# Performance work log

Hardware: AMD Instinct MI355X
Metric: run time of the kernel (lower is better)

## Reference

```python
import jax, jax.numpy as jnp
import numpy as np

B, H, W, C = 16, 32, 32, 512
NUM_HEADS = 8
ATTN_DIM = 512
HEAD_DIM = ATTN_DIM // NUM_HEADS
EPS = 1e-5


def setup_inputs() -> dict:
    key = jax.random.key(0)
    ks = jax.random.split(key, 6)
    s_in = 1.0 / np.sqrt(C)
    s_attn = 1.0 / np.sqrt(ATTN_DIM)
    return {
        "x": jax.random.normal(ks[0], (B, H, W, C), dtype=jnp.float32),
        "gamma": jnp.ones((C,), dtype=jnp.float32),
        "beta": jnp.zeros((C,), dtype=jnp.float32),
        "wq": jax.random.normal(ks[1], (C, ATTN_DIM), dtype=jnp.float32) * s_in,
        "bq": jnp.zeros((ATTN_DIM,), dtype=jnp.float32),
        "wk": jax.random.normal(ks[2], (C, ATTN_DIM), dtype=jnp.float32) * s_in,
        "bk": jnp.zeros((ATTN_DIM,), dtype=jnp.float32),
        "wv": jax.random.normal(ks[3], (C, ATTN_DIM), dtype=jnp.float32) * s_in,
        "bv": jnp.zeros((ATTN_DIM,), dtype=jnp.float32),
        "wo": jax.random.normal(ks[4], (ATTN_DIM, C), dtype=jnp.float32) * s_attn,
        "bo": jnp.zeros((C,), dtype=jnp.float32),
    }


def reference(x, gamma, beta, wq, bq, wk, bk, wv, bv, wo, bo):
    b, h, w, c = x.shape
    t = h * w  # number of spatial tokens
    # GroupNorm with 1 group: normalize over (H, W, C) per sample
    mean = jnp.mean(x, axis=(1, 2, 3), keepdims=True)
    var = jnp.var(x, axis=(1, 2, 3), keepdims=True)
    xn = (x - mean) * jax.lax.rsqrt(var + EPS) * gamma + beta
    xn = xn.reshape(b, t, c)
    # 1x1-conv q/k/v == dense over channel dim; split into heads
    q = (xn @ wq + bq).reshape(b, t, NUM_HEADS, HEAD_DIM)
    k = (xn @ wk + bk).reshape(b, t, NUM_HEADS, HEAD_DIM)
    v = (xn @ wv + bv).reshape(b, t, NUM_HEADS, HEAD_DIM)
    scale = 1.0 / jnp.sqrt(jnp.asarray(HEAD_DIM, dtype=x.dtype))
    scores = jnp.einsum('bqhd,bkhd->bhqk', q, k) * scale
    probs = jax.nn.softmax(scores, axis=-1)
    attn = jnp.einsum('bhqk,bkhd->bqhd', probs, v).reshape(b, t, ATTN_DIM)
    out = attn @ wo + bo
    # Multiplex([None, branch]): residual add, then Reshape([-1, model_dim])
    return x.reshape(b, t, c) + out
```

## Files before the change

### kernel.cpp

```cpp
#include <hip/hip_runtime.h>
#include <hip/hip_bf16.h>

typedef __attribute__((ext_vector_type(8))) short short8;
typedef __attribute__((ext_vector_type(4))) short short4v;
typedef __attribute__((ext_vector_type(4))) float f32x4;

#define B_ 16
#define T_ 1024
#define C_ 512
#define NH 8
#define HD 64

__device__ __forceinline__ short f2bf(float f) {
  union { float f; unsigned u; } v;
  v.f = f;
  unsigned r = v.u + 0x7fffu + ((v.u >> 16) & 1u);
  return (short)(r >> 16);
}

__device__ __forceinline__ short2 pack_bf2(float a, float b) {
  __hip_bfloat162 t = __float22bfloat162_rn(make_float2(a, b));
  short2 r;
  __builtin_memcpy(&r, &t, 4);
  return r;
}

__device__ __forceinline__ float fexp2(float x) {
  float r;
  asm("v_exp_f32 %0, %1" : "=v"(r) : "v"(x));
  return r;
}

__device__ __forceinline__ void gload_lds16(const short* g, short* l) {
  __builtin_amdgcn_global_load_lds(
      (const __attribute__((address_space(1))) void*)g,
      (__attribute__((address_space(3))) void*)l, 16, 0, 0);
}

__global__ __launch_bounds__(256) void stats1_kernel(const float* __restrict__ x,
                                                     float2* __restrict__ partials) {
  int chunk = blockIdx.x;
  int b = blockIdx.y;
  int tid = threadIdx.x;
  const float4* xb = (const float4*)(x + (size_t)b * 524288 + (size_t)chunk * 8192);
  float s = 0.f, s2 = 0.f;
#pragma unroll
  for (int i = 0; i < 8; i++) {
    float4 v = xb[tid + i * 256];
    s  += v.x + v.y + v.z + v.w;
    s2 += v.x * v.x + v.y * v.y + v.z * v.z + v.w * v.w;
  }
  __shared__ float ls[256], ls2[256];
  ls[tid] = s; ls2[tid] = s2;
  __syncthreads();
  for (int o = 128; o > 0; o >>= 1) {
    if (tid < o) { ls[tid] += ls[tid + o]; ls2[tid] += ls2[tid + o]; }
    __syncthreads();
  }
  if (tid == 0) partials[b * 64 + chunk] = make_float2(ls[0], ls2[0]);
}

__global__ __launch_bounds__(64) void stats2_kernel(const float2* __restrict__ partials,
                                                    float* __restrict__ stats) {
  int b = blockIdx.x;
  float2 p = partials[b * 64 + threadIdx.x];
  float s = p.x, s2 = p.y;
#pragma unroll
  for (int off = 1; off < 64; off <<= 1) {
    s  += __shfl_xor(s,  off, 64);
    s2 += __shfl_xor(s2, off, 64);
  }
  if (threadIdx.x == 0) {
    float mean = s * (1.f / 524288.f);
    float var  = s2 * (1.f / 524288.f) - mean * mean;
    stats[b * 2]     = mean;
    stats[b * 2 + 1] = rsqrtf(var + 1e-5f);
  }
}

__global__ __launch_bounds__(256) void norm_kernel(const float* __restrict__ x,
                                                   const float* __restrict__ gamma,
                                                   const float* __restrict__ beta,
                                                   const float* __restrict__ stats,
                                                   short* __restrict__ xn) {
  size_t i4 = (size_t)blockIdx.x * 256 + threadIdx.x;
  float4 v = ((const float4*)x)[i4];
  size_t i = i4 * 4;
  int b = (int)(i >> 19);
  int c = (int)(i & 511);
  float mean = stats[b * 2], rstd = stats[b * 2 + 1];
  short4v o;
  o[0] = f2bf((v.x - mean) * rstd * gamma[c + 0] + beta[c + 0]);
  o[1] = f2bf((v.y - mean) * rstd * gamma[c + 1] + beta[c + 1]);
  o[2] = f2bf((v.z - mean) * rstd * gamma[c + 2] + beta[c + 2]);
  o[3] = f2bf((v.w - mean) * rstd * gamma[c + 3] + beta[c + 3]);
  ((short4v*)xn)[i4] = o;
}

__global__ __launch_bounds__(256) void transpose_w_all(const float* __restrict__ wq,
                                                       const float* __restrict__ wk,
                                                       const float* __restrict__ wv,
                                                       const float* __restrict__ wo,
                                                       short* __restrict__ wqkvT,
                                                       short* __restrict__ woT) {
  int o = blockIdx.x * 256 + threadIdx.x;
  int sel = o >> 18;
  int oo = o & 262143;
  int k = oo >> 9, n = oo & 511;
  const float* w = (sel == 0) ? wq : (sel == 1) ? wk : (sel == 2) ? wv : wo;
  float val = w[oo];
  if (sel < 3) wqkvT[((size_t)(sel * 512 + n)) * 512 + k] = f2bf(val);
  else         woT[(size_t)n * 512 + k] = f2bf(val);
}

__global__ __launch_bounds__(256) void gemm_qkv(const short* __restrict__ A,
                                                const short* __restrict__ Bt,
                                                const float* __restrict__ bq,
                                                const float* __restrict__ bk,
                                                const float* __restrict__ bv,
                                                short* __restrict__ C) {
  __shared__ __align__(16) short As[128 * 32];
  __shared__ __align__(16) short Bs[128 * 32];
  int tid = threadIdx.x;
  int w = tid >> 6, lane = tid & 63;
  int quad = lane >> 4, l16 = lane & 15;
  int mw = (w >> 1) * 64, nw = (w & 1) * 64;
  int seg = (blockIdx.x * 128) >> 9;
  const float* bias = (seg == 0) ? bq : (seg == 1) ? bk : bv;
  float smul = (seg == 0) ? 0.18033688011112042f : 1.0f;
  const short* Atile = A + (size_t)(blockIdx.y * 128) * 512;
  const short* Btile = Bt + (size_t)(blockIdx.x * 128) * 512;
  int srow = (w << 4) + (lane >> 2);
  int scol = (lane & 3) * 8;
  f32x4 acc[4][4] = {};
  for (int k0 = 0; k0 < 512; k0 += 32) {
    __syncthreads();
    gload_lds16(&Atile[(size_t)srow * 512 + k0 + scol],        &As[w * 512]);
    gload_lds16(&Atile[(size_t)(srow + 64) * 512 + k0 + scol], &As[2048 + w * 512]);
    gload_lds16(&Btile[(size_t)srow * 512 + k0 + scol],        &Bs[w * 512]);
    gload_lds16(&Btile[(size_t)(srow + 64) * 512 + k0 + scol], &Bs[2048 + w * 512]);
    __syncthreads();
    short8 af[4], bf[4];
#pragma unroll
    for (int i = 0; i < 4; i++) af[i] = *(const short8*)(&As[(mw + i * 16 + l16) * 32 + quad * 8]);
#pragma unroll
    for (int i = 0; i < 4; i++) bf[i] = *(const short8*)(&Bs[(nw + i * 16 + l16) * 32 + quad * 8]);
#pragma unroll
    for (int mi = 0; mi < 4; mi++)
#pragma unroll
      for (int ni = 0; ni < 4; ni++)
        acc[mi][ni] = __builtin_amdgcn_mfma_f32_16x16x32_bf16(af[mi], bf[ni], acc[mi][ni], 0, 0, 0);
  }
  int m0 = blockIdx.y * 128 + mw;
  int n0 = blockIdx.x * 128 + nw;
#pragma unroll
  for (int mi = 0; mi < 4; mi++)
#pragma unroll
    for (int ni = 0; ni < 4; ni++) {
      int col = n0 + ni * 16 + l16;
      float bval = bias[col & 511];
#pragma unroll
      for (int r = 0; r < 4; r++) {
        int row = m0 + mi * 16 + quad * 4 + r;
        C[(size_t)row * 1536 + col] = f2bf((acc[mi][ni][r] + bval) * smul);
      }
    }
}

__global__ __launch_bounds__(256) void gemm_out(const short* __restrict__ A,
                                                const short* __restrict__ Bt,
                                                const float* __restrict__ bias,
                                                const float* __restrict__ xres,
                                                float* __restrict__ out) {
  __shared__ __align__(16) short As[128 * 32];
  __shared__ __align__(16) short Bs[128 * 32];
  int tid = threadIdx.x;
  int w = tid >> 6, lane = tid & 63;
  int quad = lane >> 4, l16 = lane & 15;
  int mw = (w >> 1) * 64, nw = (w & 1) * 64;
  const short* Atile = A + (size_t)(blockIdx.y * 128) * 512;
  const short* Btile = Bt + (size_t)(blockIdx.x * 128) * 512;
  int srow = (w << 4) + (lane >> 2);
  int scol = (lane & 3) * 8;
  f32x4 acc[4][4] = {};
  for (int k0 = 0; k0 < 512; k0 += 32) {
    __syncthreads();
    gload_lds16(&Atile[(size_t)srow * 512 + k0 + scol],        &As[w * 512]);
    gload_lds16(&Atile[(size_t)(srow + 64) * 512 + k0 + scol], &As[2048 + w * 512]);
    gload_lds16(&Btile[(size_t)srow * 512 + k0 + scol],        &Bs[w * 512]);
    gload_lds16(&Btile[(size_t)(srow + 64) * 512 + k0 + scol], &Bs[2048 + w * 512]);
    __syncthreads();
    short8 af[4], bf[4];
#pragma unroll
    for (int i = 0; i < 4; i++) af[i] = *(const short8*)(&As[(mw + i * 16 + l16) * 32 + quad * 8]);
#pragma unroll
    for (int i = 0; i < 4; i++) bf[i] = *(const short8*)(&Bs[(nw + i * 16 + l16) * 32 + quad * 8]);
#pragma unroll
    for (int mi = 0; mi < 4; mi++)
#pragma unroll
      for (int ni = 0; ni < 4; ni++)
        acc[mi][ni] = __builtin_amdgcn_mfma_f32_16x16x32_bf16(af[mi], bf[ni], acc[mi][ni], 0, 0, 0);
  }
  int m0 = blockIdx.y * 128 + mw;
  int n0 = blockIdx.x * 128 + nw;
#pragma unroll
  for (int mi = 0; mi < 4; mi++)
#pragma unroll
    for (int ni = 0; ni < 4; ni++) {
      int col = n0 + ni * 16 + l16;
      float bval = bias[col];
#pragma unroll
      for (int r = 0; r < 4; r++) {
        int row = m0 + mi * 16 + quad * 4 + r;
        out[(size_t)row * 512 + col] = acc[mi][ni][r] + bval + xres[(size_t)row * 512 + col];
      }
    }
}

__global__ __launch_bounds__(256) void vtrans_kernel(const short* __restrict__ qkv,
                                                     short* __restrict__ vT) {
  int chunk = blockIdx.x;
  int h  = blockIdx.y;
  int b  = blockIdx.z;
  int tid = threadIdx.x;
  __shared__ short TB[128 * 72];
  const short* src = qkv + ((size_t)b * T_ + chunk * 128) * 1536 + 1024 + (size_t)h * 64;
#pragma unroll
  for (int i = 0; i < 4; i++) {
    int idx = tid + i * 256;
    int t = idx >> 3, c = idx & 7;
    *(short8*)(&TB[t * 72 + c * 8]) = *(const short8*)(src + (size_t)t * 1536 + c * 8);
  }
  __syncthreads();
  short* dst = vT + ((size_t)(b * 8 + h) * 64) * 1024 + chunk * 128;
#pragma unroll
  for (int i = 0; i < 4; i++) {
    int idx = tid + i * 256;
    int d = idx >> 4, sc = idx & 15;
    int w2 = sc >> 2, q2 = sc & 3;
    short8 o;
#pragma unroll
    for (int sg = 0; sg < 8; sg++) {
      int half = sg >> 2, r = sg & 3;
      o[sg] = TB[(half * 64 + w2 * 16 + q2 * 4 + r) * 72 + d];
    }
    *(short8*)(dst + (size_t)d * 1024 + sc * 8) = o;
  }
}

__global__ __launch_bounds__(256) void attn_kernel(const short* __restrict__ Q,
                                                   const short* __restrict__ Kmat,
                                                   const short* __restrict__ vTg,
                                                   short* __restrict__ O) {
  int tid = threadIdx.x;
  int w = tid >> 6, lane = tid & 63;
  int quad = lane >> 4, l16 = lane & 15;
  int bh = blockIdx.x;
  int qt = blockIdx.y;
  int b = bh >> 3, h = bh & 7;
  size_t base  = ((size_t)b * T_) * 1536 + (size_t)h * 64;
  size_t vbase = ((size_t)bh * 64) * 1024;
  size_t obase = ((size_t)b * T_) * 512 + (size_t)h * 64;
  int qrow0 = qt * 64;

  __shared__ __align__(16) char smem[32768 + 1024];
  short* KTb[2];
  KTb[0] = (short*)smem;
  KTb[1] = (short*)(smem + 16384);
  float* Lbuf = (float*)smem;
  float* denomL = (float*)(smem + 32768);

  short8 qf0[4], qf1[4];
#pragma unroll
  for (int g = 0; g < 4; g++) {
    const short* qp = Q + base + (size_t)(qrow0 + g * 16 + l16) * 1536 + quad * 8;
    qf0[g] = *(const short8*)qp;
    qf1[g] = *(const short8*)(qp + 32);
  }

  const short* ksrc[4];
#pragma unroll
  for (int n = 0; n < 4; n++) {
    int bk = w * 256 + n * 64 + lane;
    int key = bk >> 3, jc = bk & 7;
    int dcol = jc ^ (key & 7);
    ksrc[n] = Kmat + base + (size_t)key * 1536 + dcol * 8;
  }

  const short* vp0 = vTg + vbase + (size_t)l16 * 1024 + (w * 4 + quad) * 8;

  int l7 = l16 & 7;
  int kA0 = ((w * 16 + l16) * 8 + (quad ^ l7)) * 8;
  int kA1 = ((w * 16 + l16) * 8 + ((quad + 4) ^ l7)) * 8;
  int kB0 = kA0 + 4096;
  int kB1 = kA1 + 4096;

  f32x4 oacc[4][4] = {};
  float lsum[4] = {0.f, 0.f, 0.f, 0.f};

#pragma unroll
  for (int n = 0; n < 4; n++)
    gload_lds16(ksrc[n], KTb[0] + (w * 256 + n * 64) * 8);

#pragma unroll
  for (int t = 0; t < 8; t++) {
    short* KTc = KTb[t & 1];
    short* KTn = KTb[(t + 1) & 1];
    __syncthreads();
    short8 vfr[4];
#pragma unroll
    for (int f = 0; f < 4; f++)
      vfr[f] = *(const short8*)(vp0 + (size_t)f * 16384 + t * 128);
    if (t < 7) {
#pragma unroll
      for (int n = 0; n < 4; n++)
        gload_lds16(ksrc[n] + (size_t)(t + 1) * 196608, KTn + (w * 256 + n * 64) * 8);
    }
    short8 ka0 = *(const short8*)(KTc + kA0);
    short8 ka1 = *(const short8*)(KTc + kA1);
    short8 kb0 = *(const short8*)(KTc + kB0);
    short8 kb1 = *(const short8*)(KTc + kB1);

#pragma unroll
    for (int g = 0; g < 4; g++) {
      f32x4 za = {}, zb = {};
      za = __builtin_amdgcn_mfma_f32_16x16x32_bf16(ka0, qf0[g], za, 0, 0, 0);
      za = __builtin_amdgcn_mfma_f32_16x16x32_bf16(ka1, qf1[g], za, 0, 0, 0);
      zb = __builtin_amdgcn_mfma_f32_16x16x32_bf16(kb0, qf0[g], zb, 0, 0, 0);
      zb = __builtin_amdgcn_mfma_f32_16x16x32_bf16(kb1, qf1[g], zb, 0, 0, 0);
      float pa0 = fexp2(za[0]), pa1 = fexp2(za[1]);
      float pa2 = fexp2(za[2]), pa3 = fexp2(za[3]);
      float pb0 = fexp2(zb[0]), pb1 = fexp2(zb[1]);
      float pb2 = fexp2(zb[2]), pb3 = fexp2(zb[3]);
      lsum[g] += (pa0 + pa1) + (pa2 + pa3) + ((pb0 + pb1) + (pb2 + pb3));
      short2 a01 = pack_bf2(pa0, pa1), a23 = pack_bf2(pa2, pa3);
      short2 b01 = pack_bf2(pb0, pb1), b23 = pack_bf2(pb2, pb3);
      short8 pf;
      pf[0] = a01.x; pf[1] = a01.y; pf[2] = a23.x; pf[3] = a23.y;
      pf[4] = b01.x; pf[5] = b01.y; pf[6] = b23.x; pf[7] = b23.y;
#pragma unroll
      for (int f = 0; f < 4; f++)
        oacc[f][g] = __builtin_amdgcn_mfma_f32_16x16x32_bf16(vfr[f], pf, oacc[f][g], 0, 0, 0);
    }
  }

#pragma unroll
  for (int g = 0; g < 4; g++) {
    lsum[g] += __shfl_xor(lsum[g], 16, 64);
    lsum[g] += __shfl_xor(lsum[g], 32, 64);
  }
  if (quad == 0) {
#pragma unroll
    for (int g = 0; g < 4; g++) denomL[w * 64 + g * 16 + l16] = lsum[g];
  }
  for (int ww = 0; ww < 4; ww++) {
    __syncthreads();
    if (w == ww) {
#pragma unroll
      for (int g = 0; g < 4; g++)
#pragma unroll
        for (int f = 0; f < 4; f++) {
          float* p = &Lbuf[(g * 16 + l16) * 68 + f * 16 + quad * 4];
          if (ww == 0) *(f32x4*)p = oacc[f][g];
          else         *(f32x4*)p = *(f32x4*)p + oacc[f][g];
        }
    }
  }
  __syncthreads();

  int q = tid >> 2, seg = tid & 3;
  float dn = denomL[q] + denomL[64 + q] + denomL[128 + q] + denomL[192 + q];
  float rinv = __frcp_rn(dn);
  const float* row = &Lbuf[q * 68 + seg * 16];
  short8 o0, o1;
#pragma unroll
  for (int i = 0; i < 8; i++) o0[i] = f2bf(row[i] * rinv);
#pragma unroll
  for (int i = 0; i < 8; i++) o1[i] = f2bf(row[8 + i] * rinv);
  short* op = O + obase + (size_t)(qrow0 + q) * 512 + seg * 16;
  *(short8*)op = o0;
  *(short8*)(op + 8) = o1;
}

extern "C" void kernel_launch(void* const* d_in, const int* in_sizes, int n_in,
                              void* d_out, int out_size, void* d_ws, size_t ws_size,
                              hipStream_t stream) {
  const float* x     = (const float*)d_in[0];
  const float* gamma = (const float*)d_in[1];
  const float* beta  = (const float*)d_in[2];
  const float* wq    = (const float*)d_in[3];
  const float* bq    = (const float*)d_in[4];
  const float* wk    = (const float*)d_in[5];
  const float* bk    = (const float*)d_in[6];
  const float* wv    = (const float*)d_in[7];
  const float* bv    = (const float*)d_in[8];
  const float* wo    = (const float*)d_in[9];
  const float* bo    = (const float*)d_in[10];
  float* out = (float*)d_out;

  char* ws = (char*)d_ws;
  const size_t XN_ELEMS = (size_t)B_ * T_ * C_;
  size_t off = 0;
  float* stats = (float*)(ws + off); off += 256;
  float2* partials = (float2*)(ws + off); off += 16 * 64 * sizeof(float2);
  short* xn    = (short*)(ws + off); off += XN_ELEMS * 2;
  short* wqkvT = (short*)(ws + off); off += (size_t)1536 * 512 * 2;
  short* woT   = (short*)(ws + off); off += (size_t)512 * 512 * 2;
  short* qkv   = (short*)(ws + off); off += (size_t)B_ * T_ * 1536 * 2;
  short* vTb   = (short*)(ws + off); off += XN_ELEMS * 2;
  short* ao    = (short*)(ws + off); off += XN_ELEMS * 2;

  stats1_kernel<<<dim3(64, 16), 256, 0, stream>>>(x, partials);
  stats2_kernel<<<16, 64, 0, stream>>>(partials, stats);
  norm_kernel<<<8192, 256, 0, stream>>>(x, gamma, beta, stats, xn);
  transpose_w_all<<<4096, 256, 0, stream>>>(wq, wk, wv, wo, wqkvT, woT);

  gemm_qkv<<<dim3(12, 128), 256, 0, stream>>>(xn, wqkvT, bq, bk, bv, qkv);

  vtrans_kernel<<<dim3(8, 8, 16), 256, 0, stream>>>(qkv, vTb);
  attn_kernel<<<dim3(128, 16), 256, 0, stream>>>(qkv, qkv + 512, vTb, ao);

  gemm_out<<<dim3(4, 128), 256, 0, stream>>>(ao, woT, bo, x, out);
}
```

Baseline: 252.7 us.

## Fuse V transpose into QKV GEMM epilogue and remap attention block order

The QKV GEMM epilogue now writes the V segment straight into the transposed per-head layout the attention kernel reads, so the separate vtrans kernel and its read/write of V go away. The Q/K buffer shrinks to a 1024-wide row stride. The attention kernel also remaps block indices so that consecutive blocks cover different heads and batches, which changes L2 locality. The V stores from the epilogue are scattered 8-byte writes, which may coalesce less well than the old transpose kernel's stores.

```diff
diff --git a/kernel.cpp b/kernel.cpp
--- a/kernel.cpp
+++ b/kernel.cpp
@@ -118,7 +118,8 @@
                                                 const float* __restrict__ bq,
                                                 const float* __restrict__ bk,
                                                 const float* __restrict__ bv,
-                                                short* __restrict__ C) {
+                                                short* __restrict__ C,
+                                                short* __restrict__ vT) {
   __shared__ __align__(16) short As[128 * 32];
   __shared__ __align__(16) short Bs[128 * 32];
   int tid = threadIdx.x;
@@ -153,18 +154,38 @@
   }
   int m0 = blockIdx.y * 128 + mw;
   int n0 = blockIdx.x * 128 + nw;
-#pragma unroll
-  for (int mi = 0; mi < 4; mi++)
-#pragma unroll
-    for (int ni = 0; ni < 4; ni++) {
-      int col = n0 + ni * 16 + l16;
-      float bval = bias[col & 511];
-#pragma unroll
-      for (int r = 0; r < 4; r++) {
-        int row = m0 + mi * 16 + quad * 4 + r;
-        C[(size_t)row * 1536 + col] = f2bf((acc[mi][ni][r] + bval) * smul);
+  if (seg < 2) {
+#pragma unroll
+    for (int mi = 0; mi < 4; mi++)
+#pragma unroll
+      for (int ni = 0; ni < 4; ni++) {
+        int col = n0 + ni * 16 + l16;
+        float bval = bias[col & 511];
+#pragma unroll
+        for (int r = 0; r < 4; r++) {
+          int row = m0 + mi * 16 + quad * 4 + r;
+          C[(size_t)row * 1024 + col] = f2bf((acc[mi][ni][r] + bval) * smul);
+        }
       }
-    }
+  } else {
+    int b = blockIdx.y >> 3;
+    int chunk = blockIdx.y & 7;
+    int half = mw >> 6;
+#pragma unroll
+    for (int mi = 0; mi < 4; mi++)
+#pragma unroll
+      for (int ni = 0; ni < 4; ni++) {
+        int c = (n0 - 1024) + ni * 16 + l16;
+        int h = c >> 6, d = c & 63;
+        float bval = bias[c];
+        short4v pk;
+#pragma unroll
+        for (int r = 0; r < 4; r++) pk[r] = f2bf(acc[mi][ni][r] + bval);
+        short* dst = vT + ((size_t)((b * 8 + h) * 64 + d)) * 1024
+                        + chunk * 128 + mi * 32 + quad * 8 + half * 4;
+        *(short4v*)dst = pk;
+      }
+  }
 }
 
 __global__ __launch_bounds__(256) void gemm_out(const short* __restrict__ A,
@@ -217,37 +238,6 @@
     }
 }
 
-__global__ __launch_bounds__(256) void vtrans_kernel(const short* __restrict__ qkv,
-                                                     short* __restrict__ vT) {
-  int chunk = blockIdx.x;
-  int h  = blockIdx.y;
-  int b  = blockIdx.z;
-  int tid = threadIdx.x;
-  __shared__ short TB[128 * 72];
-  const short* src = qkv + ((size_t)b * T_ + chunk * 128) * 1536 + 1024 + (size_t)h * 64;
-#pragma unroll
-  for (int i = 0; i < 4; i++) {
-    int idx = tid + i * 256;
-    int t = idx >> 3, c = idx & 7;
-    *(short8*)(&TB[t * 72 + c * 8]) = *(const short8*)(src + (size_t)t * 1536 + c * 8);
-  }
-  __syncthreads();
-  short* dst = vT + ((size_t)(b * 8 + h) * 64) * 1024 + chunk * 128;
-#pragma unroll
-  for (int i = 0; i < 4; i++) {
-    int idx = tid + i * 256;
-    int d = idx >> 4, sc = idx & 15;
-    int w2 = sc >> 2, q2 = sc & 3;
-    short8 o;
-#pragma unroll
-    for (int sg = 0; sg < 8; sg++) {
-      int half = sg >> 2, r = sg & 3;
-      o[sg] = TB[(half * 64 + w2 * 16 + q2 * 4 + r) * 72 + d];
-    }
-    *(short8*)(dst + (size_t)d * 1024 + sc * 8) = o;
-  }
-}
-
 __global__ __launch_bounds__(256) void attn_kernel(const short* __restrict__ Q,
                                                    const short* __restrict__ Kmat,
                                                    const short* __restrict__ vTg,
@@ -255,10 +245,11 @@
   int tid = threadIdx.x;
   int w = tid >> 6, lane = tid & 63;
   int quad = lane >> 4, l16 = lane & 15;
-  int bh = blockIdx.x;
-  int qt = blockIdx.y;
+  int lin = blockIdx.y * 128 + blockIdx.x;
+  int bh = (lin & 7) * 16 + (lin >> 7);
+  int qt = (lin >> 3) & 15;
   int b = bh >> 3, h = bh & 7;
-  size_t base  = ((size_t)b * T_) * 1536 + (size_t)h * 64;
+  size_t base  = ((size_t)b * T_) * 1024 + (size_t)h * 64;
   size_t vbase = ((size_t)bh * 64) * 1024;
   size_t obase = ((size_t)b * T_) * 512 + (size_t)h * 64;
   int qrow0 = qt * 64;
@@ -273,7 +264,7 @@
   short8 qf0[4], qf1[4];
 #pragma unroll
   for (int g = 0; g < 4; g++) {
-    const short* qp = Q + base + (size_t)(qrow0 + g * 16 + l16) * 1536 + quad * 8;
+    const short* qp = Q + base + (size_t)(qrow0 + g * 16 + l16) * 1024 + quad * 8;
     qf0[g] = *(const short8*)qp;
     qf1[g] = *(const short8*)(qp + 32);
   }
@@ -284,7 +275,7 @@
     int bk = w * 256 + n * 64 + lane;
     int key = bk >> 3, jc = bk & 7;
     int dcol = jc ^ (key & 7);
-    ksrc[n] = Kmat + base + (size_t)key * 1536 + dcol * 8;
+    ksrc[n] = Kmat + base + (size_t)key * 1024 + dcol * 8;
   }
 
   const short* vp0 = vTg + vbase + (size_t)l16 * 1024 + (w * 4 + quad) * 8;
@@ -314,7 +305,7 @@
     if (t < 7) {
 #pragma unroll
       for (int n = 0; n < 4; n++)
-        gload_lds16(ksrc[n] + (size_t)(t + 1) * 196608, KTn + (w * 256 + n * 64) * 8);
+        gload_lds16(ksrc[n] + (size_t)(t + 1) * 131072, KTn + (w * 256 + n * 64) * 8);
     }
     short8 ka0 = *(const short8*)(KTc + kA0);
     short8 ka1 = *(const short8*)(KTc + kA1);
@@ -406,7 +397,7 @@
   short* xn    = (short*)(ws + off); off += XN_ELEMS * 2;
   short* wqkvT = (short*)(ws + off); off += (size_t)1536 * 512 * 2;
   short* woT   = (short*)(ws + off); off += (size_t)512 * 512 * 2;
-  short* qkv   = (short*)(ws + off); off += (size_t)B_ * T_ * 1536 * 2;
+  short* qkv   = (short*)(ws + off); off += (size_t)B_ * T_ * 1024 * 2;
   short* vTb   = (short*)(ws + off); off += XN_ELEMS * 2;
   short* ao    = (short*)(ws + off); off += XN_ELEMS * 2;
 
@@ -415,9 +406,8 @@
   norm_kernel<<<8192, 256, 0, stream>>>(x, gamma, beta, stats, xn);
   transpose_w_all<<<4096, 256, 0, stream>>>(wq, wk, wv, wo, wqkvT, woT);
 
-  gemm_qkv<<<dim3(12, 128), 256, 0, stream>>>(xn, wqkvT, bq, bk, bv, qkv);
-
-  vtrans_kernel<<<dim3(8, 8, 16), 256, 0, stream>>>(qkv, vTb);
+  gemm_qkv<<<dim3(12, 128), 256, 0, stream>>>(xn, wqkvT, bq, bk, bv, qkv, vTb);
+
   attn_kernel<<<dim3(128, 16), 256, 0, stream>>>(qkv, qkv + 512, vTb, ao);
 
   gemm_out<<<dim3(4, 128), 256, 0, stream>>>(ao, woT, bo, x, out);
```

After: 246.7 us. 1.02x faster.
